# Performance work log

Hardware: AMD Instinct MI355X
Metric: run time of the kernel (lower is better)

## Reference

```python
import jax, jax.numpy as jnp
import numpy as np

LNC = -1000000000.0
B, K, L, V, D = 64, 8, 256, 50257, 1024
EOS, PAD = 50256, 0
LENGTH_PENALTY = 1.0
EARLY_STOPPING = False


def _gather_beams(t, idx):
    # t: (B, old_beams, ...), idx: (B, new_beams) -> (B, new_beams, ...)
    idx = idx.reshape(idx.shape + (1,) * (t.ndim - 2))
    return jnp.take_along_axis(t, idx, axis=1)


def setup_inputs() -> dict:
    key = jax.random.key(0)
    ks = jax.random.split(key, 8)
    return dict(
        input_ids=jax.random.randint(ks[0], (B * K, 1), 0, V).astype(jnp.int32),
        sequences_state=jax.random.randint(ks[1], (B, K, L), 0, V).astype(jnp.int32),
        running_sequences_state=jax.random.randint(ks[2], (B, K, L), 0, V).astype(jnp.int32),
        log_probs_state=jax.random.normal(ks[3], (B, K), jnp.float32),
        running_log_probs_state=jax.random.normal(ks[4], (B, K), jnp.float32),
        is_finished_state=jax.random.randint(ks[5], (B, K), 0, 2).astype(jnp.int32),
        embed=jax.random.normal(ks[6], (V, D), jnp.float32) * 0.02,
        W=jax.random.normal(ks[7], (D, V), jnp.float32) * 0.02,
        absolute_step=17,
    )


def reference(input_ids, sequences_state, running_sequences_state, log_probs_state,
              running_log_probs_state, is_finished_state, embed, W, absolute_step):
    step = absolute_step  # static python int (current decode position)
    # mask selecting slot 0 for the freshly fed token
    mask = jnp.zeros((B, K, L), jnp.int32).at[:, :, 0].set(1)
    padded = jnp.pad(input_ids, ((0, 0), (0, L - 1))).reshape(B, K, L)
    running_sequences = mask * padded + (1 - mask) * running_sequences_state  # (B,K,L) int32

    # model: embedding lookup + LM head GEMM on the token at step-1
    model_input_ids = running_sequences[:, :, step - 1].reshape(B * K)
    logits = embed[model_input_ids] @ W                      # (B*K, V)
    log_probs = jax.nn.log_softmax(logits, axis=-1)          # logits_processor = identity
    log_probs = log_probs.reshape(B, K, V) + running_log_probs_state[:, :, None]
    flat = log_probs.reshape(B, K * V)

    beams_to_keep = 2 * K
    topk_log_probs, topk_indices = jax.lax.top_k(flat, beams_to_keep)  # (B,2K)
    topk_beam_indices = topk_indices // V
    topk_running_sequences = _gather_beams(running_sequences, topk_beam_indices)  # (B,2K,L)
    topk_ids = (topk_indices % V).astype(jnp.int32)
    topk_sequences = topk_running_sequences.at[:, :, step].set(topk_ids)

    did_finish = topk_sequences[:, :, step] == EOS           # (B,2K) bool
    running_topk_log_probs = topk_log_probs + did_finish * LNC
    next_topk_indices = jax.lax.top_k(running_topk_log_probs, K)[1]
    next_running_sequences = _gather_beams(topk_sequences, next_topk_indices)      # (B,K,L)
    next_running_log_probs = _gather_beams(running_topk_log_probs, next_topk_indices)

    topk_log_probs = topk_log_probs / (step ** LENGTH_PENALTY)
    full = jnp.all(is_finished_state.astype(bool), axis=-1, keepdims=True) & (EARLY_STOPPING is True)
    add_penalty = (~did_finish) | full
    topk_log_probs = topk_log_probs + add_penalty * LNC

    merged_sequences = jnp.concatenate([sequences_state, topk_sequences], axis=1)      # (B,3K,L)
    merged_log_probs = jnp.concatenate([log_probs_state, topk_log_probs], axis=1)      # (B,3K)
    merged_is_finished = jnp.concatenate([is_finished_state.astype(bool), did_finish], axis=1)
    topk_merged_indices = jax.lax.top_k(merged_log_probs, K)[1]
    next_sequences = _gather_beams(merged_sequences, topk_merged_indices)
    next_log_probs = _gather_beams(merged_log_probs, topk_merged_indices)
    next_is_finished = _gather_beams(merged_is_finished, topk_merged_indices)

    not_max_length_yet = step < L
    worst_finished = jnp.where(jnp.any(next_is_finished, axis=1),
                               jnp.min(log_probs_state, axis=1),
                               jnp.full((B,), LNC, jnp.float32))
    best_running = running_log_probs_state[:, 0] / (step ** LENGTH_PENALTY)
    improvement = jnp.any(best_running > worst_finished)
    still_open = ~(jnp.all(next_is_finished) & (EARLY_STOPPING is True))
    continue_search = not_max_length_yet & still_open & improvement

    none_finished = jnp.any(next_is_finished, axis=1)
    seqs = jnp.where(none_finished[:, None, None], next_sequences, next_running_sequences)
    generated_tokens = seqs[:, 0]                 # (B, L)
    done = ~continue_search
    return generated_tokens, done, next_log_probs, next_running_log_probs
```

## Files before the change

kernel.cpp:

```cpp
#include <hip/hip_runtime.h>
#include <cstdint>
#include <cstddef>

#define BB 64
#define KK 8
#define LL 256
#define VV 50257
#define DD 1024
#define EOS_TOK 50256
#define LNCf (-1000000000.0f)
#define NT 393
#define NCOL 50304
#define MAXT 400

typedef unsigned short ushort_t;
typedef __attribute__((ext_vector_type(4))) float f32x4;
typedef __attribute__((ext_vector_type(8))) _Float16 f16x8;

struct __attribute__((packed, aligned(4))) f4u { float x, y, z, w; };

__device__ inline unsigned f16_rne(float x) {
    _Float16 h = (_Float16)x;
    return (unsigned)*(ushort_t*)&h;
}

__global__ __launch_bounds__(256) void conv_aw(
    const float* __restrict__ embed, const int* __restrict__ input_ids,
    const int* __restrict__ rss, const int* __restrict__ step_p,
    ushort_t* __restrict__ At, const float* __restrict__ W,
    ushort_t* __restrict__ Wt)
{
    const int bx = blockIdx.x;
    const int t = threadIdx.x;

    if (bx < 512) {
        const int r = bx;
        const int step = *step_p;
        const int tok = (step == 1) ? input_ids[r] : rss[r * LL + (step - 1)];
        f32x4 v = *(const f32x4*)(embed + (size_t)tok * DD + t * 4);
        ushort4 h;
        h.x = (ushort_t)f16_rne(v[0]); h.y = (ushort_t)f16_rne(v[1]);
        h.z = (ushort_t)f16_rne(v[2]); h.w = (ushort_t)f16_rne(v[3]);
        *(ushort4*)(At + (size_t)r * DD + t * 4) = h;
        return;
    }

    const int b2 = bx - 512;
    const int kt = b2 & 15;
    const int nt2 = b2 >> 4;
    const int k0 = kt * 64;
    const int n0 = nt2 * 128;

    const int ko = t & 7;
    const int nq = t >> 3;
    const int kbase = k0 + ko * 8;
    const int nbase = n0 + nq * 4;

    float x[8][4];
    const bool full = (nbase + 3 < VV);
#pragma unroll
    for (int j = 0; j < 8; ++j) {
        const float* wp = W + (size_t)(kbase + j) * VV + nbase;
        if (full) {
            f4u u = *(const f4u*)wp;
            x[j][0] = u.x; x[j][1] = u.y; x[j][2] = u.z; x[j][3] = u.w;
        } else {
#pragma unroll
            for (int i = 0; i < 4; ++i)
                x[j][i] = (nbase + i < VV) ? wp[i] : 0.f;
        }
    }
#pragma unroll
    for (int i = 0; i < 4; ++i) {
        uint4 o;
        o.x = f16_rne(x[0][i]) | (f16_rne(x[1][i]) << 16);
        o.y = f16_rne(x[2][i]) | (f16_rne(x[3][i]) << 16);
        o.z = f16_rne(x[4][i]) | (f16_rne(x[5][i]) << 16);
        o.w = f16_rne(x[6][i]) | (f16_rne(x[7][i]) << 16);
        *(uint4*)(Wt + (size_t)(nbase + i) * DD + kbase) = o;
    }
}

__global__ __launch_bounds__(256) void gemm_full(
    const ushort_t* __restrict__ At, const ushort_t* __restrict__ Wt,
    float* __restrict__ logits, float* __restrict__ msum2)
{
    __shared__ ushort_t smem[16384];
    ushort_t* Ah = smem;
    ushort_t* Bs = smem + 8192;

    const int tid = threadIdx.x;
    const int wave = tid >> 6;
    const int lane = tid & 63;
    const int i = blockIdx.x;
    const int m_t = (i >> 3) & 3;
    const int n_t = (i & 7) + (((i >> 3) >> 2) << 3);
    if (n_t >= NT) return;
    const int m0 = m_t * 128;
    const int wm = wave >> 1, wn = wave & 1;
    const int fr = lane & 15;
    const int q  = lane >> 4;

    const int srow = lane >> 3;
    const int schunk = lane & 7;

    f32x4 acc[4][4];
#pragma unroll
    for (int a = 0; a < 4; ++a)
#pragma unroll
        for (int b = 0; b < 4; ++b)
#pragma unroll
            for (int e = 0; e < 4; ++e) acc[a][b][e] = 0.f;

    for (int t7 = 0; t7 < 16; ++t7) {
        const int kb = t7 * 64;
#pragma unroll
        for (int ii = 0; ii < 4; ++ii) {
            const int row = (ii * 4 + wave) * 8 + srow;
            const int soff = (schunk ^ (row & 7)) * 8;
            const ushort_t* srcA = At + (size_t)(m0 + row) * DD + kb + soff;
            const ushort_t* srcB = Wt + (size_t)(n_t * 128 + row) * DD + kb + soff;
            __builtin_amdgcn_global_load_lds(
                (const __attribute__((address_space(1))) unsigned int*)srcA,
                (__attribute__((address_space(3))) unsigned int*)(Ah + (ii * 4 + wave) * 512),
                16, 0, 0);
            __builtin_amdgcn_global_load_lds(
                (const __attribute__((address_space(1))) unsigned int*)srcB,
                (__attribute__((address_space(3))) unsigned int*)(Bs + (ii * 4 + wave) * 512),
                16, 0, 0);
        }
        __syncthreads();
#pragma unroll
        for (int h = 0; h < 2; ++h) {
            f16x8 b[4];
#pragma unroll
            for (int fn = 0; fn < 4; ++fn) {
                const int row = wn * 64 + fn * 16 + fr;
                const int off = ((h * 4 + q) ^ (row & 7)) * 16;
                b[fn] = *(const f16x8*)((const char*)(Bs + row * 64) + off);
            }
#pragma unroll
            for (int fm = 0; fm < 4; ++fm) {
                const int row = wm * 64 + fm * 16 + fr;
                const int off = ((h * 4 + q) ^ (row & 7)) * 16;
                f16x8 a = *(const f16x8*)((const char*)(Ah + row * 64) + off);
#pragma unroll
                for (int fn = 0; fn < 4; ++fn)
                    acc[fm][fn] = __builtin_amdgcn_mfma_f32_16x16x32_f16(a, b[fn], acc[fm][fn], 0, 0, 0);
            }
        }
        __syncthreads();
    }

    const int n0 = n_t * 128;
    if (n0 + 128 > VV) {
        const int cgb = n0 + wn * 64 + fr;
#pragma unroll
        for (int fn = 0; fn < 4; ++fn)
            if (cgb + fn * 16 >= VV) {
#pragma unroll
                for (int fm = 0; fm < 4; ++fm)
#pragma unroll
                    for (int e = 0; e < 4; ++e) acc[fm][fn][e] = -INFINITY;
            }
    }

    const int crow0 = m0 + wm * 64 + q * 4;
    const int ccol0 = n0 + wn * 64 + fr;
#pragma unroll
    for (int fm = 0; fm < 4; ++fm)
#pragma unroll
        for (int fn = 0; fn < 4; ++fn) {
            const int col = ccol0 + fn * 16;
#pragma unroll
            for (int e = 0; e < 4; ++e)
                logits[(size_t)(crow0 + fm * 16 + e) * NCOL + col] = acc[fm][fn][e];
        }

#pragma unroll
    for (int fm = 0; fm < 4; ++fm)
#pragma unroll
        for (int e = 0; e < 4; ++e) {
            const float v0 = acc[fm][0][e], v1 = acc[fm][1][e];
            const float v2 = acc[fm][2][e], v3 = acc[fm][3][e];
            float vm = fmaxf(fmaxf(v0, v1), fmaxf(v2, v3));
#pragma unroll
            for (int sh = 1; sh < 16; sh <<= 1) vm = fmaxf(vm, __shfl_xor(vm, sh, 64));
            float vs = __expf(v0 - vm) + __expf(v1 - vm) + __expf(v2 - vm) + __expf(v3 - vm);
#pragma unroll
            for (int sh = 1; sh < 16; sh <<= 1) vs += __shfl_xor(vs, sh, 64);
            if (fr == 0) {
                const int row = m0 + wm * 64 + fm * 16 + q * 4 + e;
                float2 p; p.x = vm; p.y = vs;
                *(float2*)&msum2[((size_t)row * NT + n_t) * 4 + wn * 2] = p;
            }
        }
}

__global__ __launch_bounds__(256) void prune_topk(
    const float* __restrict__ msum2, const float* __restrict__ logits,
    float* __restrict__ lse_out, float* __restrict__ tv_out,
    int* __restrict__ ti_out)
{
    const int r = blockIdx.x;
    const int tid = threadIdx.x;

    __shared__ int s_tlist[MAXT];
    __shared__ int s_cnt;

    if (tid < 64) {
        const int lane = tid;
        float m = -INFINITY, s = 0.f;
        float tv[16]; int tvi[16];
#pragma unroll
        for (int j = 0; j < 16; ++j) { tv[j] = -INFINITY; tvi[j] = 0x7fffffff; }

        for (int p = lane; p < NT; p += 64) {
            const f32x4 qv = *(const f32x4*)&msum2[((size_t)r * NT + p) * 4];
            float mm = fmaxf(m, qv[0]);
            s = s * __expf(m - mm) + qv[1] * __expf(qv[0] - mm);
            m = mm;
            mm = fmaxf(m, qv[2]);
            s = s * __expf(m - mm) + qv[3] * __expf(qv[2] - mm);
            m = mm;
            const float tmax = fmaxf(qv[0], qv[2]);
            if (tmax > tv[15]) {
                float cv = tmax; int ci = p;
#pragma unroll
                for (int j = 0; j < 16; ++j) {
                    const bool sw = (cv > tv[j]);
                    const float tf = tv[j]; const int ti2 = tvi[j];
                    if (sw) { tv[j] = cv; tvi[j] = ci; cv = tf; ci = ti2; }
                }
            }
        }
#pragma unroll
        for (int sh = 1; sh < 64; sh <<= 1) {
            const float m2 = __shfl_xor(m, sh, 64), s2 = __shfl_xor(s, sh, 64);
            const float mm = fmaxf(m, m2);
            s = s * __expf(m - mm) + s2 * __expf(m2 - mm);
            m = mm;
        }
        if (lane == 0) lse_out[r] = m + logf(s);

        unsigned used = 0;
        float T = -INFINITY;
#pragma unroll
        for (int t = 0; t < 16; ++t) {
            float bv = -INFINITY; int bi = 0x7fffffff;
#pragma unroll
            for (int j = 0; j < 16; ++j) {
                if (!((used >> j) & 1u) &&
                    (tv[j] > bv || (tv[j] == bv && tvi[j] < bi))) { bv = tv[j]; bi = tvi[j]; }
            }
#pragma unroll
            for (int sh = 1; sh < 64; sh <<= 1) {
                const float v2 = __shfl_xor(bv, sh, 64);
                const int i2 = __shfl_xor(bi, sh, 64);
                if (v2 > bv || (v2 == bv && i2 < bi)) { bv = v2; bi = i2; }
            }
#pragma unroll
            for (int j = 0; j < 16; ++j)
                if (tvi[j] == bi) used |= 1u << j;
            T = bv;
        }

        const unsigned long long lmask_lt = (1ULL << lane) - 1ULL;
        int base = 0;
        for (int it = 0; it < 7; ++it) {
            const int p = it * 64 + lane;
            bool pred = false;
            if (p < NT) {
                const f32x4 qv = *(const f32x4*)&msum2[((size_t)r * NT + p) * 4];
                pred = fmaxf(qv[0], qv[2]) >= T;
            }
            const unsigned long long mask = __ballot(pred);
            if (pred) s_tlist[base + __popcll(mask & lmask_lt)] = p;
            base += __popcll(mask);
        }
        if (lane == 0) s_cnt = base;
    }
    __syncthreads();

    const int cnt = s_cnt;
    float v[16]; int id[16];
#pragma unroll
    for (int j = 0; j < 16; ++j) { v[j] = -INFINITY; id[j] = 0x7fffffff; }

    const int total = cnt * 128;
    for (int idx = tid; idx < total; idx += 256) {
        const int tile = s_tlist[idx >> 7];
        const int col = tile * 128 + (idx & 127);
        const float x = logits[(size_t)r * NCOL + col];
        if (x > v[15] || (x == v[15] && col < id[15])) {
            float cv = x; int ci = col;
#pragma unroll
            for (int j = 0; j < 16; ++j) {
                const bool sw = (cv > v[j]) || (cv == v[j] && ci < id[j]);
                const float tf = v[j]; const int ti2 = id[j];
                if (sw) { v[j] = cv; id[j] = ci; cv = tf; ci = ti2; }
            }
        }
    }

    __shared__ float mvv[256][17];
    __shared__ int mii[256][17];
#pragma unroll
    for (int j = 0; j < 16; ++j) { mvv[tid][j] = v[j]; mii[tid][j] = id[j]; }
    __syncthreads();

    auto level = [&](int st) {
        float nv[16]; int ni2[16];
        const float* av = mvv[tid];      const int* ai = mii[tid];
        const float* bv = mvv[tid + st]; const int* bi = mii[tid + st];
        int pa = 0, pb = 0;
#pragma unroll
        for (int o = 0; o < 16; ++o) {
            const float va = av[pa], vb2 = bv[pb];
            const int ia = ai[pa], ib = bi[pb];
            const bool ta = (va > vb2) || (va == vb2 && ia < ib);
            nv[o] = ta ? va : vb2;
            ni2[o] = ta ? ia : ib;
            pa += ta ? 1 : 0;
            pb += ta ? 0 : 1;
        }
#pragma unroll
        for (int j = 0; j < 16; ++j) { mvv[tid][j] = nv[j]; mii[tid][j] = ni2[j]; }
    };

    if (tid < 128) level(128);
    __syncthreads();
    if (tid < 64) {
        level(64); level(32); level(16); level(8); level(4); level(2); level(1);
        if (tid < 16) {
            tv_out[r * 16 + tid] = mvv[0][tid];
            ti_out[r * 16 + tid] = mii[0][tid];
        }
    }
}

__global__ __launch_bounds__(64) void beam_logic(
    const float* __restrict__ lse, const float* __restrict__ tv,
    const int* __restrict__ ti, const int* __restrict__ input_ids,
    const int* __restrict__ seq_state, const int* __restrict__ rss,
    const float* __restrict__ lps, const float* __restrict__ rlps,
    const int* __restrict__ isfin, const int* __restrict__ step_p,
    float* __restrict__ out, int* __restrict__ improve_ws,
    unsigned* __restrict__ ticket)
{
    const int b = blockIdx.x;
    const int lane = threadIdx.x;
    const int kk = lane >> 3;
    const int r = b * KK + kk;

    const float off_r = rlps[r] - lse[r];

    const int s0 = (lane & 7) * 2;
    float cv[2]; int cidx[2];
#pragma unroll
    for (int mq = 0; mq < 2; ++mq) {
        cv[mq] = tv[r * 16 + s0 + mq] + off_r;
        cidx[mq] = kk * VV + ti[r * 16 + s0 + mq];
    }

    float wv[16]; int wi[16];
#pragma unroll
    for (int t = 0; t < 16; ++t) {
        float bv = cv[0]; int bi = cidx[0];
        if (cv[1] > bv || (cv[1] == bv && cidx[1] < bi)) { bv = cv[1]; bi = cidx[1]; }
#pragma unroll
        for (int sh = 1; sh < 64; sh <<= 1) {
            const float v2 = __shfl_xor(bv, sh, 64);
            const int i2 = __shfl_xor(bi, sh, 64);
            if (v2 > bv || (v2 == bv && i2 < bi)) { bv = v2; bi = i2; }
        }
        wv[t] = bv; wi[t] = bi;
#pragma unroll
        for (int mq = 0; mq < 2; ++mq)
            if (cidx[mq] == bi) { cv[mq] = -INFINITY; cidx[mq] = 0x7fffffff; }
    }

    int mode = 0, beam = 0, selk = 0, selv = 0, step = 0;
    if (lane == 0) {
        step = *step_p;
        const float stepf = (float)step;
        float runtl[16]; int tkk[16], tkid[16]; unsigned finmask = 0;
#pragma unroll
        for (int j = 0; j < 16; ++j) {
            tkk[j] = wi[j] / VV;
            tkid[j] = wi[j] - tkk[j] * VV;
            const bool f = (tkid[j] == EOS_TOK);
            finmask |= (f ? 1u : 0u) << j;
            runtl[j] = wv[j] + (f ? LNCf : 0.f);
        }
        unsigned used = 0;
        int selk_run = 0, selv_run = 0;
#pragma unroll
        for (int i2 = 0; i2 < 8; ++i2) {
            float bvv = 0.f; int bj = -1, bk = 0, bv2 = 0;
#pragma unroll
            for (int j = 0; j < 16; ++j) {
                if (!((used >> j) & 1u) && (bj < 0 || runtl[j] > bvv)) {
                    bvv = runtl[j]; bj = j; bk = tkk[j]; bv2 = tkid[j];
                }
            }
            used |= 1u << bj;
            out[BB * LL + 1 + BB * KK + b * KK + i2] = bvv;
            if (i2 == 0) { selk_run = bk; selv_run = bv2; }
        }
        float mvx[24]; unsigned mfinmask = 0;
#pragma unroll
        for (int j = 0; j < 8; ++j) {
            mvx[j] = lps[b * KK + j];
            mfinmask |= ((isfin[b * KK + j] != 0) ? 1u : 0u) << j;
        }
#pragma unroll
        for (int j = 0; j < 16; ++j) {
            const bool f = (finmask >> j) & 1u;
            mvx[8 + j] = wv[j] / stepf + (f ? 0.f : LNCf);
            mfinmask |= (f ? 1u : 0u) << (8 + j);
        }
        unsigned used2 = 0; int anyf = 0;
        int m0_state = 0, m0_beam = 0, m0_k = 0, m0_v = 0;
#pragma unroll
        for (int i2 = 0; i2 < 8; ++i2) {
            float bvv = 0.f; int bj = -1, bf = 0, bstate = 0, bbeam = 0, bk = 0, bv2 = 0;
#pragma unroll
            for (int j = 0; j < 24; ++j) {
                if (!((used2 >> j) & 1u) && (bj < 0 || mvx[j] > bvv)) {
                    bvv = mvx[j]; bj = j; bf = (mfinmask >> j) & 1u;
                    bstate = (j < 8) ? 1 : 0; bbeam = j;
                    bk = (j < 8) ? 0 : tkk[j - 8]; bv2 = (j < 8) ? 0 : tkid[j - 8];
                }
            }
            used2 |= 1u << bj;
            out[BB * LL + 1 + b * KK + i2] = bvv;
            anyf |= bf;
            if (i2 == 0) { m0_state = bstate; m0_beam = bbeam; m0_k = bk; m0_v = bv2; }
        }
        float worst = LNCf;
        if (anyf) {
            worst = lps[b * KK];
#pragma unroll
            for (int j = 1; j < 8; ++j) worst = fminf(worst, lps[b * KK + j]);
        }
        improve_ws[b] = ((rlps[b * KK] / stepf) > worst) ? 1 : 0;
        if (anyf) {
            if (m0_state) { mode = 0; beam = m0_beam; }
            else { mode = 1; selk = m0_k; selv = m0_v; }
        } else {
            mode = 1; selk = selk_run; selv = selv_run;
        }
    }
    mode = __shfl(mode, 0, 64);
    beam = __shfl(beam, 0, 64);
    selk = __shfl(selk, 0, 64);
    selv = __shfl(selv, 0, 64);
    step = __shfl(step, 0, 64);

#pragma unroll
    for (int it = 0; it < 4; ++it) {
        const int t2 = it * 64 + lane;
        int tokv;
        if (mode == 0) {
            tokv = seq_state[(b * KK + beam) * LL + t2];
        } else {
            tokv = (t2 == step) ? selv
                 : ((t2 == 0) ? input_ids[b * KK + selk]
                              : rss[(b * KK + selk) * LL + t2]);
        }
        out[b * LL + t2] = (float)tokv;
    }

    __threadfence();
    if (lane == 0) {
        const unsigned slot = atomicAdd(ticket, 1u);
        if ((slot & 63u) == 63u) {
            __threadfence();
            int any = 0;
#pragma unroll
            for (int j = 0; j < BB; ++j) any |= improve_ws[j];
            const bool cont = (step < LL) && (any != 0);
            out[BB * LL] = cont ? 0.f : 1.f;
        }
    }
}

extern "C" void kernel_launch(void* const* d_in, const int* in_sizes, int n_in,
                              void* d_out, int out_size, void* d_ws, size_t ws_size,
                              hipStream_t stream) {
    const int*   input_ids = (const int*)d_in[0];
    const int*   seq_state = (const int*)d_in[1];
    const int*   rss       = (const int*)d_in[2];
    const float* lps       = (const float*)d_in[3];
    const float* rlps      = (const float*)d_in[4];
    const int*   isfin     = (const int*)d_in[5];
    const float* embed     = (const float*)d_in[6];
    const float* W         = (const float*)d_in[7];
    const int*   step_p    = (const int*)d_in[8];
    float* out = (float*)d_out;

    char* ws = (char*)d_ws;
    size_t off = 0;
    auto alloc = [&](size_t bytes) { void* p = ws + off; off += (bytes + 255) & ~(size_t)255; return p; };
    ushort_t* Wt     = (ushort_t*)alloc((size_t)NCOL * DD * 2);
    float*    logits = (float*)alloc((size_t)512 * NCOL * 4);
    ushort_t* At     = (ushort_t*)alloc((size_t)512 * DD * 2);
    float*    msum2  = (float*)alloc((size_t)512 * NT * 4 * 4);
    float*    lse    = (float*)alloc(512 * 4);
    float*    tvals  = (float*)alloc(512 * 16 * 4);
    int*      tidx   = (int*)alloc(512 * 16 * 4);
    int*      improw = (int*)alloc(64 * 4);
    unsigned* ticket = (unsigned*)alloc(4);
    (void)ws_size; (void)in_sizes; (void)n_in; (void)out_size;

    conv_aw<<<512 + 16 * 393, 256, 0, stream>>>(embed, input_ids, rss, step_p,
                                                At, W, Wt);
    gemm_full<<<1600, 256, 0, stream>>>(At, Wt, logits, msum2);
    prune_topk<<<512, 256, 0, stream>>>(msum2, logits, lse, tvals, tidx);
    beam_logic<<<64, 64, 0, stream>>>(lse, tvals, tidx, input_ids, seq_state,
                                      rss, lps, rlps, isfin, step_p, out,
                                      improw, ticket);
}
```

Measured before the change: 250.1 us.

## Fuse fp32-to-fp16 weight conversion into GEMM B-tile loading

Removes the separate pass that converted W to a transposed fp16 copy in workspace. The GEMM now loads fp32 W tiles directly, converts them to fp16 in registers and writes them swizzled into LDS. This removes one full write and re-read of the converted weight matrix. In exchange, each m-tile block rereads fp32 W and the B loads are no longer asynchronous global-to-LDS copies.

```diff
diff --git a/kernel.cpp b/kernel.cpp
--- a/kernel.cpp
+++ b/kernel.cpp
@@ -24,65 +24,24 @@
     return (unsigned)*(ushort_t*)&h;
 }
 
-__global__ __launch_bounds__(256) void conv_aw(
+__global__ __launch_bounds__(256) void conv_a(
     const float* __restrict__ embed, const int* __restrict__ input_ids,
     const int* __restrict__ rss, const int* __restrict__ step_p,
-    ushort_t* __restrict__ At, const float* __restrict__ W,
-    ushort_t* __restrict__ Wt)
+    ushort_t* __restrict__ At)
 {
-    const int bx = blockIdx.x;
+    const int r = blockIdx.x;
     const int t = threadIdx.x;
-
-    if (bx < 512) {
-        const int r = bx;
-        const int step = *step_p;
-        const int tok = (step == 1) ? input_ids[r] : rss[r * LL + (step - 1)];
-        f32x4 v = *(const f32x4*)(embed + (size_t)tok * DD + t * 4);
-        ushort4 h;
-        h.x = (ushort_t)f16_rne(v[0]); h.y = (ushort_t)f16_rne(v[1]);
-        h.z = (ushort_t)f16_rne(v[2]); h.w = (ushort_t)f16_rne(v[3]);
-        *(ushort4*)(At + (size_t)r * DD + t * 4) = h;
-        return;
-    }
-
-    const int b2 = bx - 512;
-    const int kt = b2 & 15;
-    const int nt2 = b2 >> 4;
-    const int k0 = kt * 64;
-    const int n0 = nt2 * 128;
-
-    const int ko = t & 7;
-    const int nq = t >> 3;
-    const int kbase = k0 + ko * 8;
-    const int nbase = n0 + nq * 4;
-
-    float x[8][4];
-    const bool full = (nbase + 3 < VV);
-#pragma unroll
-    for (int j = 0; j < 8; ++j) {
-        const float* wp = W + (size_t)(kbase + j) * VV + nbase;
-        if (full) {
-            f4u u = *(const f4u*)wp;
-            x[j][0] = u.x; x[j][1] = u.y; x[j][2] = u.z; x[j][3] = u.w;
-        } else {
-#pragma unroll
-            for (int i = 0; i < 4; ++i)
-                x[j][i] = (nbase + i < VV) ? wp[i] : 0.f;
-        }
-    }
-#pragma unroll
-    for (int i = 0; i < 4; ++i) {
-        uint4 o;
-        o.x = f16_rne(x[0][i]) | (f16_rne(x[1][i]) << 16);
-        o.y = f16_rne(x[2][i]) | (f16_rne(x[3][i]) << 16);
-        o.z = f16_rne(x[4][i]) | (f16_rne(x[5][i]) << 16);
-        o.w = f16_rne(x[6][i]) | (f16_rne(x[7][i]) << 16);
-        *(uint4*)(Wt + (size_t)(nbase + i) * DD + kbase) = o;
-    }
+    const int step = *step_p;
+    const int tok = (step == 1) ? input_ids[r] : rss[r * LL + (step - 1)];
+    f32x4 v = *(const f32x4*)(embed + (size_t)tok * DD + t * 4);
+    ushort4 h;
+    h.x = (ushort_t)f16_rne(v[0]); h.y = (ushort_t)f16_rne(v[1]);
+    h.z = (ushort_t)f16_rne(v[2]); h.w = (ushort_t)f16_rne(v[3]);
+    *(ushort4*)(At + (size_t)r * DD + t * 4) = h;
 }
 
 __global__ __launch_bounds__(256) void gemm_full(
-    const ushort_t* __restrict__ At, const ushort_t* __restrict__ Wt,
+    const ushort_t* __restrict__ At, const float* __restrict__ W,
     float* __restrict__ logits, float* __restrict__ msum2)
 {
     __shared__ ushort_t smem[16384];
@@ -104,6 +63,11 @@
     const int srow = lane >> 3;
     const int schunk = lane & 7;
 
+    const int nq = tid & 31;
+    const int ko = tid >> 5;
+    const int nb = n_t * 128 + nq * 4;
+    const bool bfull = (nb + 3 < VV);
+
     f32x4 acc[4][4];
 #pragma unroll
     for (int a = 0; a < 4; ++a)
@@ -119,15 +83,36 @@
             const int row = (ii * 4 + wave) * 8 + srow;
             const int soff = (schunk ^ (row & 7)) * 8;
             const ushort_t* srcA = At + (size_t)(m0 + row) * DD + kb + soff;
-            const ushort_t* srcB = Wt + (size_t)(n_t * 128 + row) * DD + kb + soff;
             __builtin_amdgcn_global_load_lds(
                 (const __attribute__((address_space(1))) unsigned int*)srcA,
                 (__attribute__((address_space(3))) unsigned int*)(Ah + (ii * 4 + wave) * 512),
                 16, 0, 0);
-            __builtin_amdgcn_global_load_lds(
-                (const __attribute__((address_space(1))) unsigned int*)srcB,
-                (__attribute__((address_space(3))) unsigned int*)(Bs + (ii * 4 + wave) * 512),
-                16, 0, 0);
+        }
+        {
+            float x[8][4];
+#pragma unroll
+            for (int j = 0; j < 8; ++j) {
+                const int krow = kb + ko * 8 + j;
+                const float* wp = W + (size_t)krow * VV + nb;
+                if (bfull) {
+                    f4u u = *(const f4u*)wp;
+                    x[j][0] = u.x; x[j][1] = u.y; x[j][2] = u.z; x[j][3] = u.w;
+                } else {
+#pragma unroll
+                    for (int ii = 0; ii < 4; ++ii)
+                        x[j][ii] = (nb + ii < VV) ? wp[ii] : 0.f;
+                }
+            }
+#pragma unroll
+            for (int ii = 0; ii < 4; ++ii) {
+                const int n = nq * 4 + ii;
+                uint4 o;
+                o.x = f16_rne(x[0][ii]) | (f16_rne(x[1][ii]) << 16);
+                o.y = f16_rne(x[2][ii]) | (f16_rne(x[3][ii]) << 16);
+                o.z = f16_rne(x[4][ii]) | (f16_rne(x[5][ii]) << 16);
+                o.w = f16_rne(x[6][ii]) | (f16_rne(x[7][ii]) << 16);
+                *(uint4*)((char*)Bs + n * 128 + ((ko ^ (n & 7)) * 16)) = o;
+            }
         }
         __syncthreads();
 #pragma unroll
@@ -503,7 +488,6 @@
     char* ws = (char*)d_ws;
     size_t off = 0;
     auto alloc = [&](size_t bytes) { void* p = ws + off; off += (bytes + 255) & ~(size_t)255; return p; };
-    ushort_t* Wt     = (ushort_t*)alloc((size_t)NCOL * DD * 2);
     float*    logits = (float*)alloc((size_t)512 * NCOL * 4);
     ushort_t* At     = (ushort_t*)alloc((size_t)512 * DD * 2);
     float*    msum2  = (float*)alloc((size_t)512 * NT * 4 * 4);
@@ -514,9 +498,8 @@
     unsigned* ticket = (unsigned*)alloc(4);
     (void)ws_size; (void)in_sizes; (void)n_in; (void)out_size;
 
-    conv_aw<<<512 + 16 * 393, 256, 0, stream>>>(embed, input_ids, rss, step_p,
-                                                At, W, Wt);
-    gemm_full<<<1600, 256, 0, stream>>>(At, Wt, logits, msum2);
+    conv_a<<<512, 256, 0, stream>>>(embed, input_ids, rss, step_p, At);
+    gemm_full<<<1600, 256, 0, stream>>>(At, W, logits, msum2);
     prune_topk<<<512, 256, 0, stream>>>(msum2, logits, lse, tvals, tidx);
     beam_logic<<<64, 64, 0, stream>>>(lse, tvals, tidx, input_ids, seq_state,
                                       rss, lps, rlps, isfin, step_p, out,
```

Result: slower. 353.4 us (+41.3%).
